# Kernel optimization log

Hardware: AMD Instinct MI355X
Metric: run time of the kernel (lower is better)

Reference implementation:

```python
import jax, jax.numpy as jnp
import numpy as np

NUM_SEM, MAXPP, FS, FG, H, ITERS, ETN, GROUPS = 24, 10, 128, 128, 128, 2, 4, 16
N_NODES, N_EDGES = 20000, 320000


def _leaky(x):
    return jax.nn.leaky_relu(x, 0.01)


def _lin_init(k, din, dout):
    kw, kb = jax.random.split(k)
    lim = 1.0 / np.sqrt(din)
    w = jax.random.uniform(kw, (dout, din), jnp.float32, -lim, lim)
    b = jax.random.uniform(kb, (dout,), jnp.float32, -lim, lim)
    return w, b


def setup_inputs() -> dict:
    key = jax.random.key(0)
    ks = jax.random.split(key, 16)
    inp = {}
    inp["child_feats"] = jax.random.normal(ks[0], (1, N_NODES, NUM_SEM + MAXPP + FS), jnp.float32)
    inp["child_geo_feats"] = jax.random.normal(ks[1], (1, N_NODES, FG), jnp.float32)
    inp["child_exists"] = jnp.ones((1, N_NODES, 1), jnp.float32)
    inp["edge_type_onehot"] = jax.random.uniform(ks[2], (1, N_EDGES, ETN), jnp.float32)
    inp["edge_indices"] = jax.random.randint(ks[3], (1, N_EDGES, 2), 0, N_NODES)
    inp["child_op_w"], inp["child_op_b"] = _lin_init(ks[4], NUM_SEM + MAXPP + FS, H)
    inp["second_w"], inp["second_b"] = _lin_init(ks[5], H * (ITERS + 1), FS)
    ew, eb = zip(*[_lin_init(ks[6 + i], 2 * H + ETN, H) for i in range(ITERS)])
    inp["edge_w"] = jnp.stack(ew)
    inp["edge_b"] = jnp.stack(eb)
    inp["child_geo_w"], inp["child_geo_b"] = _lin_init(ks[10], FG, H)
    inp["second_geo_w"], inp["second_geo_b"] = _lin_init(ks[11], H, FG)
    inp["gn_w"] = jnp.ones((FG,), jnp.float32)
    inp["gn_b"] = jnp.zeros((FG,), jnp.float32)
    inp["skip_w"], inp["skip_b"] = _lin_init(ks[12], FG, FG)
    return inp


def _group_norm(x, w, b, groups=GROUPS, eps=1e-5):
    # x: [B, C]  (torch GroupNorm on 2D input)
    B, C = x.shape
    xg = x.reshape(B, groups, C // groups)
    mu = xg.mean(axis=-1, keepdims=True)
    var = xg.var(axis=-1, keepdims=True)
    xn = ((xg - mu) * jax.lax.rsqrt(var + eps)).reshape(B, C)
    return xn * w + b


def reference(child_feats, child_geo_feats, child_exists, edge_type_onehot, edge_indices,
              child_op_w, child_op_b, second_w, second_b, edge_w, edge_b,
              child_geo_w, child_geo_b, second_geo_w, second_geo_b, gn_w, gn_b, skip_w, skip_b):
    B, N, _ = child_feats.shape
    # struct branch
    cf = (child_feats @ child_op_w.T + child_op_b) * child_exists  # [B,N,H]
    iter_parent_feats = [cf.max(axis=1)]                           # symmetric_type='max'
    idx_from = edge_indices[0, :, 0]
    idx_to = edge_indices[0, :, 1]
    ef = edge_type_onehot[0]                                       # [E,ETN]
    for i in range(ITERS):
        # gather endpoints, concat edge type, edge-MLP + leaky relu
        msg = jnp.concatenate([cf[0, idx_from], cf[0, idx_to], ef], axis=1)  # [E,2H+ETN]
        msg = _leaky(msg @ edge_w[i].T + edge_b[i])                          # [E,H]
        # scatter_max into zero-initialized node slots (matches torch_scatter with out=zeros)
        cf = jnp.zeros((N, H), msg.dtype).at[idx_from].max(msg)[None]        # [1,N,H]
        iter_parent_feats.append(cf.max(axis=1))
    parent_feat = _leaky(jnp.concatenate(iter_parent_feats, axis=1) @ second_w.T + second_b)
    # geo branch
    skip = (child_geo_feats @ skip_w.T + skip_b) * child_exists    # [B,N,FG]
    cg = (child_geo_feats @ child_geo_w.T + child_geo_b) * child_exists  # [B,N,H]
    pg = _leaky(cg.max(axis=1))
    sg = _leaky(skip.max(axis=1))
    parent_geo_feat = _leaky(sg + _group_norm(pg @ second_geo_w.T + second_geo_b, gn_w, gn_b))
    return parent_feat, parent_geo_feat
```

## Files before the change

kernel.cpp:

```cpp
#include <hip/hip_runtime.h>

#define N_NODES 20000
#define N_EDGES 320000
#define HD 128
#define FIN 162
#define KE 260
#define KPAD 288
#define KOP 192
#define WSTR 296
#define OSTR 200
#define GSTR 136
#define TSTR 136
#define XSTR 72

typedef unsigned short u16;
typedef __attribute__((ext_vector_type(8))) short bf16x8;
typedef __attribute__((ext_vector_type(4))) float f32x4;

__device__ __forceinline__ float leaky(float x){ return x > 0.f ? x : 0.01f*x; }
__device__ __forceinline__ unsigned fmap(float f){
    unsigned u = __float_as_uint(f);
    return (u & 0x80000000u) ? ~u : (u | 0x80000000u);
}
__device__ __forceinline__ float funmap(unsigned u){
    return __uint_as_float((u & 0x80000000u) ? (u & 0x7fffffffu) : ~u);
}
__device__ __forceinline__ unsigned umax_(unsigned a, unsigned b){ return a > b ? a : b; }
__device__ __forceinline__ u16 f2bf(float x){
    unsigned b = __float_as_uint(x);
    return (u16)((b + 0x7fffu + ((b >> 16) & 1u)) >> 16);
}
__device__ __forceinline__ float bf2f(u16 u){
    return __uint_as_float(((unsigned)u) << 16);
}

#define PB_W 16
#define PB_F 960
#define PB_G 640
#define PB_H 320
#define PREP_GRID (PB_W + PB_F + PB_G + PB_H)

__global__ __launch_bounds__(256) void prep(
    const float* __restrict__ edge_w, u16* __restrict__ Wb,
    const float* __restrict__ op_w,   u16* __restrict__ Wop,
    const float* __restrict__ geo_w,  u16* __restrict__ Wgeo,
    const float* __restrict__ skip_w, u16* __restrict__ Wskip,
    const float* __restrict__ feats,  u16* __restrict__ featsb,
    const float* __restrict__ geof,   u16* __restrict__ geob,
    const int* __restrict__ eidx, int* __restrict__ count)
{
    const int b = blockIdx.x, t = threadIdx.x;
    if (b < PB_W) {
        for (int idx = b * 256 + t; idx < 16384; idx += PB_W * 256) {
            union { u16 us[8]; uint4 v; } pk;
            if (idx < 9216) {
                int layer = idx / 4608, rem = idx - layer * 4608;
                int h = rem / 36, j = rem - h * 36;
                const float* src = edge_w + (size_t)layer * 128 * KE + h * KE;
                #pragma unroll
                for (int kk = 0; kk < 8; ++kk) {
                    int k = j * 8 + kk;
                    pk.us[kk] = (k < KE) ? f2bf(src[k]) : (u16)0;
                }
                ((uint4*)Wb)[(size_t)layer * 128 * 36 + h * 36 + j] = pk.v;
            } else if (idx < 12288) {
                int rem = idx - 9216;
                int h = rem / 24, j = rem - h * 24;
                const float* src = op_w + h * FIN;
                #pragma unroll
                for (int kk = 0; kk < 8; ++kk) {
                    int k = j * 8 + kk;
                    pk.us[kk] = (k < FIN) ? f2bf(src[k]) : (u16)0;
                }
                ((uint4*)Wop)[h * 24 + j] = pk.v;
            } else {
                int rem = idx - 12288;
                int which = rem >> 11;
                int r2 = rem & 2047;
                const float4* src = (const float4*)((which ? skip_w : geo_w)) + r2 * 2;
                float4 a = src[0], c = src[1];
                pk.us[0]=f2bf(a.x); pk.us[1]=f2bf(a.y); pk.us[2]=f2bf(a.z); pk.us[3]=f2bf(a.w);
                pk.us[4]=f2bf(c.x); pk.us[5]=f2bf(c.y); pk.us[6]=f2bf(c.z); pk.us[7]=f2bf(c.w);
                ((uint4*)(which ? Wskip : Wgeo))[r2] = pk.v;
            }
        }
    } else if (b < PB_W + PB_F) {
        for (int f = (b - PB_W) * 256 + t; f < N_NODES * 24; f += PB_F * 256) {
            int n = f / 24, j = f - n * 24;
            union { u16 us[8]; uint4 v; } pk;
            if (j < 20) {
                const float2* src = (const float2*)(feats + (size_t)n * FIN + j * 8);
                float2 p0 = src[0], p1 = src[1], p2 = src[2], p3 = src[3];
                pk.us[0]=f2bf(p0.x); pk.us[1]=f2bf(p0.y); pk.us[2]=f2bf(p1.x); pk.us[3]=f2bf(p1.y);
                pk.us[4]=f2bf(p2.x); pk.us[5]=f2bf(p2.y); pk.us[6]=f2bf(p3.x); pk.us[7]=f2bf(p3.y);
            } else if (j == 20) {
                float2 p = *(const float2*)(feats + (size_t)n * FIN + 160);
                pk.us[0]=f2bf(p.x); pk.us[1]=f2bf(p.y);
                pk.us[2]=pk.us[3]=pk.us[4]=pk.us[5]=pk.us[6]=pk.us[7]=0;
            } else {
                #pragma unroll
                for (int kk = 0; kk < 8; ++kk) pk.us[kk] = 0;
            }
            ((uint4*)featsb)[(size_t)n * 24 + j] = pk.v;
        }
    } else if (b < PB_W + PB_F + PB_G) {
        for (int g = (b - PB_W - PB_F) * 256 + t; g < N_NODES * 16; g += PB_G * 256) {
            const float4* s = (const float4*)geof + (size_t)g * 2;
            float4 a = s[0], c = s[1];
            union { u16 us[8]; uint4 v; } pk;
            pk.us[0]=f2bf(a.x); pk.us[1]=f2bf(a.y); pk.us[2]=f2bf(a.z); pk.us[3]=f2bf(a.w);
            pk.us[4]=f2bf(c.x); pk.us[5]=f2bf(c.y); pk.us[6]=f2bf(c.z); pk.us[7]=f2bf(c.w);
            ((uint4*)geob)[g] = pk.v;
        }
    } else {
        for (int e = (b - PB_W - PB_F - PB_G) * 256 + t; e < N_EDGES; e += PB_H * 256)
            atomicAdd(&count[eidx[2 * e]], 1);
    }
}

__global__ __launch_bounds__(1024) void scan_offsets(
    const int* __restrict__ count, int* __restrict__ offset)
{
    __shared__ int part[1024];
    const int t = threadIdx.x;
    const int lo = t * 20;
    const int hi = min(lo + 20, N_NODES);
    int s = 0;
    for (int n = lo; n < hi; ++n) s += count[n];
    part[t] = s;
    __syncthreads();
    for (int d = 1; d < 1024; d <<= 1) {
        int v = (t >= d) ? part[t - d] : 0;
        __syncthreads();
        part[t] += v;
        __syncthreads();
    }
    int run = (t > 0) ? part[t - 1] : 0;
    for (int n = lo; n < hi; ++n) { offset[n] = run; run += count[n]; }
}

__global__ __launch_bounds__(256) void mid(
    const int* __restrict__ eidx, const float* __restrict__ ef,
    const int* __restrict__ offset, int* __restrict__ cursor,
    int* __restrict__ from_p, int* __restrict__ to_p, uint2* __restrict__ efb_p,
    const u16* __restrict__ featsb, const u16* __restrict__ geob,
    const float* __restrict__ exists,
    const u16* __restrict__ Wop, const float* __restrict__ op_b,
    const u16* __restrict__ Wgeo, const float* __restrict__ geo_b,
    const u16* __restrict__ Wskip, const float* __restrict__ skip_b,
    u16* __restrict__ cf_a,
    unsigned* __restrict__ ipf0_m, unsigned* __restrict__ pg_m,
    unsigned* __restrict__ sg_m)
{
    __shared__ __align__(16) u16 smem[128 * OSTR];
    __shared__ float ex_s[128];
    __shared__ unsigned colmax_s[128];

    const int blk = blockIdx.x, t = threadIdx.x;
    if (blk < 1250) {
        int e = blk * 256 + t;
        int2 p = ((const int2*)eidx)[e];
        int pos = offset[p.x] + atomicAdd(&cursor[p.x], 1);
        from_p[pos] = p.x; to_p[pos] = p.y;
        float4 e4 = ((const float4*)ef)[e];
        efb_p[pos] = make_uint2(
            (unsigned)f2bf(e4.x) | ((unsigned)f2bf(e4.y) << 16),
            (unsigned)f2bf(e4.z) | ((unsigned)f2bf(e4.w) << 16));
        return;
    }
    const int b = blk - 1250;
    const int mode = (b < 157) ? 0 : (b < 314) ? 1 : 2;
    const int bx = b - (mode == 0 ? 0 : mode == 1 ? 157 : 314);
    const int base = bx * 128;
    const int wave = t >> 6, l = t & 63;
    const int quad = l >> 4, lc = l & 15;
    const int R0 = (wave >> 1) * 64;
    const int C0 = (wave & 1) * 64;

    const u16* W = (mode == 0) ? Wop : (mode == 1) ? Wgeo : Wskip;
    const float* bias = (mode == 0) ? op_b : (mode == 1) ? geo_b : skip_b;
    unsigned* accout = (mode == 0) ? ipf0_m : (mode == 1) ? pg_m : sg_m;
    const int KW = (mode == 0) ? KOP : HD;
    const int SW = (mode == 0) ? OSTR : GSTR;
    const int NCH = (mode == 0) ? 6 : 4;
    const u16* A = (mode == 0) ? featsb : geob;

    {
        const int r = t >> 1, half = t & 1;
        const int nu4 = KW / 16;
        const uint4* src = (const uint4*)(W + (size_t)r * KW) + half * nu4;
        uint4* dst = (uint4*)(smem + r * SW) + half * nu4;
        for (int i = 0; i < nu4; ++i) dst[i] = src[i];
    }
    if (t < 128) {
        int n = base + t; if (n >= N_NODES) n = N_NODES - 1;
        ex_s[t] = exists[n];
        colmax_s[t] = 0u;
    }
    __syncthreads();

    f32x4 acc[4][4];
    #pragma unroll
    for (int i = 0; i < 4; ++i)
        #pragma unroll
        for (int j = 0; j < 4; ++j) acc[i][j] = (f32x4){0.f, 0.f, 0.f, 0.f};

    int nd[4];
    #pragma unroll
    for (int ti = 0; ti < 4; ++ti) {
        int n = base + R0 + ti * 16 + lc;
        nd[ti] = (n < N_NODES) ? n : N_NODES - 1;
    }

    for (int c = 0; c < NCH; ++c) {
        bf16x8 af[4], bfr[4];
        #pragma unroll
        for (int ti = 0; ti < 4; ++ti)
            af[ti] = *(const bf16x8*)(A + (size_t)nd[ti] * KW + c * 32 + quad * 8);
        #pragma unroll
        for (int tj = 0; tj < 4; ++tj)
            bfr[tj] = *(const bf16x8*)(smem + (C0 + tj * 16 + lc) * SW + c * 32 + quad * 8);
        #pragma unroll
        for (int ti = 0; ti < 4; ++ti)
            #pragma unroll
            for (int tj = 0; tj < 4; ++tj)
                acc[ti][tj] = __builtin_amdgcn_mfma_f32_16x16x32_bf16(
                    af[ti], bfr[tj], acc[ti][tj], 0, 0, 0);
    }

    #pragma unroll
    for (int tj = 0; tj < 4; ++tj) {
        const int col = C0 + tj * 16 + lc;
        const float bc = bias[col];
        unsigned mx = 0u;
        #pragma unroll
        for (int ti = 0; ti < 4; ++ti) {
            #pragma unroll
            for (int r = 0; r < 4; ++r) {
                int row = R0 + ti * 16 + quad * 4 + r;
                float x = (acc[ti][tj][r] + bc) * ex_s[row];
                acc[ti][tj][r] = x;
                mx = umax_(mx, fmap(x));
            }
        }
        atomicMax(&colmax_s[col], mx);
    }
    __syncthreads();
    if (t < 128) atomicMax(&accout[t], colmax_s[t]);

    if (mode == 0) {
        #pragma unroll
        for (int ti = 0; ti < 4; ++ti)
            #pragma unroll
            for (int tj = 0; tj < 4; ++tj) {
                const int col = C0 + tj * 16 + lc;
                #pragma unroll
                for (int r = 0; r < 4; ++r)
                    smem[(R0 + ti * 16 + quad * 4 + r) * TSTR + col] = f2bf(acc[ti][tj][r]);
            }
        __syncthreads();
        #pragma unroll
        for (int i = 0; i < 8; ++i) {
            int idx = t + i * 256;
            int row = idx >> 4, c16 = idx & 15;
            int n = base + row;
            if (n < N_NODES) {
                uint4 v = *(const uint4*)(smem + row * TSTR + c16 * 8);
                *(uint4*)(cf_a + (size_t)n * HD + c16 * 8) = v;
            }
        }
    }
}

template<int REDUCE>
__global__ __launch_bounds__(512, 4) void edge_mfma(
    const u16* __restrict__ cfb,
    const int* __restrict__ from_p,
    const int* __restrict__ to_p,
    const uint2* __restrict__ efb_p,
    const u16* __restrict__ Wb,
    const float* __restrict__ bias,
    const int* __restrict__ offs,
    const int* __restrict__ cnt,
    u16* __restrict__ cf_bb,
    float* __restrict__ cf_b32,
    int* __restrict__ ipf_out)
{
    __shared__ __align__(16) u16 smem[64 * WSTR];
    __shared__ int colmax_s[64];

    const int t    = threadIdx.x;
    const int tile = blockIdx.x >> 1;
    const int half = blockIdx.x & 1;
    const int base = tile * 512;
    const int wave = t >> 6, l = t & 63;
    const int quad = l >> 4, lc = l & 15;
    const int R0 = wave * 64;
    const int C0 = half * 64;

    for (int idx = t; idx < 64 * 36; idx += 512) {
        int r = idx / 36, j = idx - r * 36;
        ((uint4*)(smem + r * WSTR))[j] = ((const uint4*)(Wb + (size_t)(C0 + r) * KPAD))[j];
    }
    if (t < 64) colmax_s[t] = 0;

    int nf[4], nt[4]; uint2 efr[4];
    #pragma unroll
    for (int ti = 0; ti < 4; ++ti) {
        int e = base + R0 + ti * 16 + lc;
        nf[ti]  = from_p[e];
        nt[ti]  = to_p[e];
        efr[ti] = efb_p[e];
    }
    __syncthreads();

    f32x4 acc[4][4];
    #pragma unroll
    for (int i = 0; i < 4; ++i)
        #pragma unroll
        for (int j = 0; j < 4; ++j) acc[i][j] = (f32x4){0.f, 0.f, 0.f, 0.f};

    #pragma unroll
    for (int c = 0; c < 8; ++c) {
        bf16x8 af[4], bfr[4];
        #pragma unroll
        for (int ti = 0; ti < 4; ++ti) {
            int node = (c < 4) ? nf[ti] : nt[ti];
            af[ti] = *(const bf16x8*)(cfb + node * HD + (c & 3) * 32 + quad * 8);
        }
        #pragma unroll
        for (int tj = 0; tj < 4; ++tj)
            bfr[tj] = *(const bf16x8*)(smem + (tj * 16 + lc) * WSTR + c * 32 + quad * 8);
        #pragma unroll
        for (int ti = 0; ti < 4; ++ti)
            #pragma unroll
            for (int tj = 0; tj < 4; ++tj)
                acc[ti][tj] = __builtin_amdgcn_mfma_f32_16x16x32_bf16(
                    af[ti], bfr[tj], acc[ti][tj], 0, 0, 0);
    }
    {
        bf16x8 af[4], bfr[4];
        #pragma unroll
        for (int ti = 0; ti < 4; ++ti) {
            union { bf16x8 v; unsigned u[4]; } p;
            p.u[0] = efr[ti].x; p.u[1] = efr[ti].y; p.u[2] = 0u; p.u[3] = 0u;
            union { bf16x8 v; unsigned u[4]; } z;
            z.u[0] = z.u[1] = z.u[2] = z.u[3] = 0u;
            af[ti] = (quad == 0) ? p.v : z.v;
        }
        #pragma unroll
        for (int tj = 0; tj < 4; ++tj)
            bfr[tj] = *(const bf16x8*)(smem + (tj * 16 + lc) * WSTR + 8 * 32 + quad * 8);
        #pragma unroll
        for (int ti = 0; ti < 4; ++ti)
            #pragma unroll
            for (int tj = 0; tj < 4; ++tj)
                acc[ti][tj] = __builtin_amdgcn_mfma_f32_16x16x32_bf16(
                    af[ti], bfr[tj], acc[ti][tj], 0, 0, 0);
    }

    #pragma unroll
    for (int tj = 0; tj < 4; ++tj) {
        const int cl = tj * 16 + lc;
        const float bc = bias[C0 + cl];
        float mx = 0.f;
        #pragma unroll
        for (int ti = 0; ti < 4; ++ti) {
            #pragma unroll
            for (int r = 0; r < 4; ++r) {
                float x = leaky(acc[ti][tj][r] + bc);
                acc[ti][tj][r] = x;
                mx = fmaxf(mx, x);
            }
        }
        atomicMax(&colmax_s[cl], __float_as_int(mx));
    }
    __syncthreads();
    if (t < 64) atomicMax(&ipf_out[C0 + t], colmax_s[t]);

    if (REDUCE) {
        const int ch = t & 63;
        #pragma unroll
        for (int ph = 0; ph < 2; ++ph) {
            if ((R0 >> 8) == ph) {
                const int rb = R0 & 255;
                #pragma unroll
                for (int ti = 0; ti < 4; ++ti)
                    #pragma unroll
                    for (int tj = 0; tj < 4; ++tj) {
                        const int cl = tj * 16 + lc;
                        #pragma unroll
                        for (int r = 0; r < 4; ++r)
                            smem[(rb + ti * 16 + quad * 4 + r) * XSTR + cl]
                                = f2bf(acc[ti][tj][r]);
                    }
            }
            __syncthreads();
            const int wb = base + ph * 256;
            const int nfirst = from_p[wb];
            const int nlast  = from_p[wb + 255];
            for (int n = nfirst + (t >> 6); n <= nlast; n += 8) {
                int o = offs[n], c = cnt[n];
                int lo = o - wb, hi = o + c - wb;
                int lo2 = lo > 0 ? lo : 0;
                int hi2 = hi < 256 ? hi : 256;
                if (lo2 >= hi2) continue;
                float m = 0.f;
                for (int r = lo2; r < hi2; ++r)
                    m = fmaxf(m, bf2f(smem[r * XSTR + ch]));
                if (lo >= 0 && hi <= 256)
                    cf_bb[(size_t)n * HD + C0 + ch] = f2bf(m);
                else
                    atomicMax((int*)&cf_b32[(size_t)n * HD + C0 + ch], __float_as_int(m));
            }
            __syncthreads();
        }
    }
}

__global__ __launch_bounds__(256) void fixup(
    const int* __restrict__ offs, const int* __restrict__ cnt,
    const float* __restrict__ cf_b32, u16* __restrict__ cf_bb)
{
    const int n = blockIdx.x * 2 + (threadIdx.x >> 7);
    const int ch = threadIdx.x & 127;
    int o = offs[n], c = cnt[n];
    if (c > 0 && (o >> 8) != ((o + c - 1) >> 8))
        cf_bb[(size_t)n * HD + ch] = f2bf(cf_b32[(size_t)n * HD + ch]);
}

__global__ __launch_bounds__(128) void heads(
    const unsigned* __restrict__ ipf0_m,
    const float* __restrict__ ipf1, const float* __restrict__ ipf2,
    const float* __restrict__ secW, const float* __restrict__ secB,
    const unsigned* __restrict__ pg_m, const unsigned* __restrict__ sg_m,
    const float* __restrict__ geoW, const float* __restrict__ geoB,
    const float* __restrict__ gnw, const float* __restrict__ gnb,
    float* __restrict__ out)
{
    const int t = threadIdx.x;
    if (blockIdx.x == 0) {
        __shared__ float s[384];
        s[t]       = funmap(ipf0_m[t]);
        s[128 + t] = ipf1[t];
        s[256 + t] = ipf2[t];
        __syncthreads();
        float acc = secB[t];
        #pragma unroll 4
        for (int k = 0; k < 384; ++k) acc = fmaf(s[k], secW[t*384 + k], acc);
        out[t] = leaky(acc);
    } else {
        __shared__ float pg[128];
        __shared__ float tt[128];
        pg[t] = leaky(funmap(pg_m[t]));
        float sg = leaky(funmap(sg_m[t]));
        __syncthreads();
        float acc = geoB[t];
        #pragma unroll 4
        for (int k = 0; k < 128; ++k) acc = fmaf(pg[k], geoW[t*128 + k], acc);
        tt[t] = acc;
        __syncthreads();
        const int g = (t >> 3) << 3;
        float mu = 0.f, m2 = 0.f;
        #pragma unroll
        for (int q = 0; q < 8; ++q) { float x = tt[g + q]; mu += x; m2 += x*x; }
        mu *= 0.125f;
        m2 = m2 * 0.125f - mu * mu;
        float xn = (acc - mu) * rsqrtf(m2 + 1e-5f);
        out[128 + t] = leaky(sg + xn * gnw[t] + gnb[t]);
    }
}

extern "C" void kernel_launch(void* const* d_in, const int* in_sizes, int n_in,
                              void* d_out, int out_size, void* d_ws, size_t ws_size,
                              hipStream_t stream)
{
    const float* child_feats  = (const float*)d_in[0];
    const float* child_geo    = (const float*)d_in[1];
    const float* child_exists = (const float*)d_in[2];
    const float* etoh         = (const float*)d_in[3];
    const int*   eidx         = (const int*)  d_in[4];
    const float* op_w   = (const float*)d_in[5];
    const float* op_b   = (const float*)d_in[6];
    const float* sec_w  = (const float*)d_in[7];
    const float* sec_b  = (const float*)d_in[8];
    const float* edge_w = (const float*)d_in[9];
    const float* edge_b = (const float*)d_in[10];
    const float* geo_w  = (const float*)d_in[11];
    const float* geo_b  = (const float*)d_in[12];
    const float* sgeo_w = (const float*)d_in[13];
    const float* sgeo_b = (const float*)d_in[14];
    const float* gn_w   = (const float*)d_in[15];
    const float* gn_b   = (const float*)d_in[16];
    const float* skip_w = (const float*)d_in[17];
    const float* skip_b = (const float*)d_in[18];
    float* out = (float*)d_out;

    char* ws = (char*)d_ws;
    size_t off = 0;
    u16*   cf_a   = (u16*)(ws + off);   off += (size_t)N_NODES*HD*2;
    u16*   featsb = (u16*)(ws + off);   off += (size_t)N_NODES*KOP*2;
    u16*   geob   = (u16*)(ws + off);   off += (size_t)N_NODES*HD*2;
    u16*   Wb     = (u16*)(ws + off);   off += (size_t)2*128*KPAD*2;
    u16*   Wop    = (u16*)(ws + off);   off += (size_t)128*KOP*2;
    u16*   Wgeo   = (u16*)(ws + off);   off += (size_t)128*128*2;
    u16*   Wskip  = (u16*)(ws + off);   off += (size_t)128*128*2;
    int*   from_p = (int*)(ws + off);   off += (size_t)N_EDGES*4;
    int*   to_p   = (int*)(ws + off);   off += (size_t)N_EDGES*4;
    uint2* efb_p  = (uint2*)(ws + off); off += (size_t)N_EDGES*8;
    int*   offs   = (int*)(ws + off);   off += (size_t)N_NODES*4;
    char*  zero0  = ws + off;
    u16*   cf_bb  = (u16*)(ws + off);         off += (size_t)N_NODES*HD*2;
    float* cf_b32 = (float*)(ws + off);       off += (size_t)N_NODES*HD*4;
    unsigned* ipf0_m = (unsigned*)(ws + off); off += 128*4;
    float*    ipf1   = (float*)(ws + off);    off += 128*4;
    float*    ipf2   = (float*)(ws + off);    off += 128*4;
    unsigned* pg_m   = (unsigned*)(ws + off); off += 128*4;
    unsigned* sg_m   = (unsigned*)(ws + off); off += 128*4;
    int*      count  = (int*)(ws + off);      off += (size_t)N_NODES*4;
    int*      cursor = (int*)(ws + off);      off += (size_t)N_NODES*4;
    size_t zero_bytes = (size_t)(ws + off - zero0);

    hipMemsetAsync(zero0, 0, zero_bytes, stream);

    prep<<<PREP_GRID, 256, 0, stream>>>(
        edge_w, Wb, op_w, Wop, geo_w, Wgeo, skip_w, Wskip,
        child_feats, featsb, child_geo, geob, eidx, count);

    scan_offsets<<<1, 1024, 0, stream>>>(count, offs);

    mid<<<1721, 256, 0, stream>>>(
        eidx, etoh, offs, cursor, from_p, to_p, efb_p,
        featsb, geob, child_exists, Wop, op_b, Wgeo, geo_b, Wskip, skip_b,
        cf_a, ipf0_m, pg_m, sg_m);

    edge_mfma<1><<<2 * (N_EDGES/512), 512, 0, stream>>>(
        cf_a, from_p, to_p, efb_p, Wb, edge_b,
        offs, count, cf_bb, cf_b32, (int*)ipf1);

    fixup<<<N_NODES/2, 256, 0, stream>>>(offs, count, cf_b32, cf_bb);

    edge_mfma<0><<<2 * (N_EDGES/512), 512, 0, stream>>>(
        cf_bb, from_p, to_p, efb_p, Wb + 128*KPAD, edge_b + 128,
        offs, count, nullptr, nullptr, (int*)ipf2);

    heads<<<2, 128, 0, stream>>>(ipf0_m, ipf1, ipf2, sec_w, sec_b,
                                 pg_m, sg_m, sgeo_w, sgeo_b, gn_w, gn_b, out);
}
```

Baseline: 294.8 us.

## Compute all 128 output columns per edge block and fold bias into GEMM

Each edge block now computes the full 128 output channels instead of splitting them across two half-blocks, so gathered node rows are loaded and used for MFMA once instead of twice. The bias is folded into the weight matrix as an extra K column, matched by a constant 1.0 in the edge-type fragment, which removes the per-column bias load and add. The scatter-max staging buffer is transposed to channel-major with packed bf16 conversion stores. The trade-off is twice the accumulator registers and shared memory per block, with the occupancy hint lowered from 4 to 2 blocks.

```diff
diff --git a/kernel.cpp b/kernel.cpp
--- a/kernel.cpp
+++ b/kernel.cpp
@@ -11,13 +11,13 @@
 #define OSTR 200
 #define GSTR 136
 #define TSTR 136
-#define XSTR 72
+#define RSTR 260
 
 typedef unsigned short u16;
 typedef __attribute__((ext_vector_type(8))) short bf16x8;
 typedef __attribute__((ext_vector_type(4))) float f32x4;
 
-__device__ __forceinline__ float leaky(float x){ return x > 0.f ? x : 0.01f*x; }
+__device__ __forceinline__ float leaky(float x){ return fmaxf(x, 0.01f*x); }
 __device__ __forceinline__ unsigned fmap(float f){
     unsigned u = __float_as_uint(f);
     return (u & 0x80000000u) ? ~u : (u | 0x80000000u);
@@ -32,6 +32,11 @@
 }
 __device__ __forceinline__ float bf2f(u16 u){
     return __uint_as_float(((unsigned)u) << 16);
+}
+__device__ __forceinline__ unsigned cvt_pk_bf16(float lo, float hi){
+    unsigned r;
+    asm("v_cvt_pk_bf16_f32 %0, %1, %2" : "=v"(r) : "v"(lo), "v"(hi));
+    return r;
 }
 
 #define PB_W 16
@@ -41,7 +46,8 @@
 #define PREP_GRID (PB_W + PB_F + PB_G + PB_H)
 
 __global__ __launch_bounds__(256) void prep(
-    const float* __restrict__ edge_w, u16* __restrict__ Wb,
+    const float* __restrict__ edge_w, const float* __restrict__ edge_bias,
+    u16* __restrict__ Wb,
     const float* __restrict__ op_w,   u16* __restrict__ Wop,
     const float* __restrict__ geo_w,  u16* __restrict__ Wgeo,
     const float* __restrict__ skip_w, u16* __restrict__ Wskip,
@@ -60,7 +66,9 @@
                 #pragma unroll
                 for (int kk = 0; kk < 8; ++kk) {
                     int k = j * 8 + kk;
-                    pk.us[kk] = (k < KE) ? f2bf(src[k]) : (u16)0;
+                    pk.us[kk] = (k < KE) ? f2bf(src[k])
+                              : (k == 260) ? f2bf(edge_bias[layer * 128 + h])
+                              : (u16)0;
                 }
                 ((uint4*)Wb)[(size_t)layer * 128 * 36 + h * 36 + j] = pk.v;
             } else if (idx < 12288) {
@@ -273,36 +281,32 @@
 }
 
 template<int REDUCE>
-__global__ __launch_bounds__(512, 4) void edge_mfma(
+__global__ __launch_bounds__(512, 2) void edge_mfma(
     const u16* __restrict__ cfb,
     const int* __restrict__ from_p,
     const int* __restrict__ to_p,
     const uint2* __restrict__ efb_p,
     const u16* __restrict__ Wb,
-    const float* __restrict__ bias,
     const int* __restrict__ offs,
     const int* __restrict__ cnt,
     u16* __restrict__ cf_bb,
     float* __restrict__ cf_b32,
     int* __restrict__ ipf_out)
 {
-    __shared__ __align__(16) u16 smem[64 * WSTR];
-    __shared__ int colmax_s[64];
+    __shared__ __align__(16) u16 smem[128 * WSTR];
+    __shared__ int colmax_s[128];
 
     const int t    = threadIdx.x;
-    const int tile = blockIdx.x >> 1;
-    const int half = blockIdx.x & 1;
-    const int base = tile * 512;
+    const int base = blockIdx.x * 512;
     const int wave = t >> 6, l = t & 63;
     const int quad = l >> 4, lc = l & 15;
     const int R0 = wave * 64;
-    const int C0 = half * 64;
-
-    for (int idx = t; idx < 64 * 36; idx += 512) {
+
+    for (int idx = t; idx < 128 * 36; idx += 512) {
         int r = idx / 36, j = idx - r * 36;
-        ((uint4*)(smem + r * WSTR))[j] = ((const uint4*)(Wb + (size_t)(C0 + r) * KPAD))[j];
-    }
-    if (t < 64) colmax_s[t] = 0;
+        ((uint4*)(smem + r * WSTR))[j] = ((const uint4*)(Wb + (size_t)r * KPAD))[j];
+    }
+    if (t < 128) colmax_s[t] = 0;
 
     int nf[4], nt[4]; uint2 efr[4];
     #pragma unroll
@@ -314,61 +318,62 @@
     }
     __syncthreads();
 
-    f32x4 acc[4][4];
+    f32x4 acc[4][8];
     #pragma unroll
     for (int i = 0; i < 4; ++i)
         #pragma unroll
-        for (int j = 0; j < 4; ++j) acc[i][j] = (f32x4){0.f, 0.f, 0.f, 0.f};
+        for (int j = 0; j < 8; ++j) acc[i][j] = (f32x4){0.f, 0.f, 0.f, 0.f};
 
     #pragma unroll
     for (int c = 0; c < 8; ++c) {
-        bf16x8 af[4], bfr[4];
+        bf16x8 af[4], bfr[8];
         #pragma unroll
         for (int ti = 0; ti < 4; ++ti) {
             int node = (c < 4) ? nf[ti] : nt[ti];
             af[ti] = *(const bf16x8*)(cfb + node * HD + (c & 3) * 32 + quad * 8);
         }
         #pragma unroll
-        for (int tj = 0; tj < 4; ++tj)
+        for (int tj = 0; tj < 8; ++tj)
             bfr[tj] = *(const bf16x8*)(smem + (tj * 16 + lc) * WSTR + c * 32 + quad * 8);
         #pragma unroll
         for (int ti = 0; ti < 4; ++ti)
             #pragma unroll
-            for (int tj = 0; tj < 4; ++tj)
+            for (int tj = 0; tj < 8; ++tj)
                 acc[ti][tj] = __builtin_amdgcn_mfma_f32_16x16x32_bf16(
                     af[ti], bfr[tj], acc[ti][tj], 0, 0, 0);
     }
     {
-        bf16x8 af[4], bfr[4];
+        bf16x8 af[4], bfr[8];
         #pragma unroll
         for (int ti = 0; ti < 4; ++ti) {
             union { bf16x8 v; unsigned u[4]; } p;
-            p.u[0] = efr[ti].x; p.u[1] = efr[ti].y; p.u[2] = 0u; p.u[3] = 0u;
+            p.u[0] = efr[ti].x; p.u[1] = efr[ti].y;
+            p.u[2] = 0x00003f80u;
+            p.u[3] = 0u;
             union { bf16x8 v; unsigned u[4]; } z;
             z.u[0] = z.u[1] = z.u[2] = z.u[3] = 0u;
             af[ti] = (quad == 0) ? p.v : z.v;
         }
         #pragma unroll
-        for (int tj = 0; tj < 4; ++tj)
+        for (int tj = 0; tj < 8; ++tj)
             bfr[tj] = *(const bf16x8*)(smem + (tj * 16 + lc) * WSTR + 8 * 32 + quad * 8);
         #pragma unroll
         for (int ti = 0; ti < 4; ++ti)
             #pragma unroll
-            for (int tj = 0; tj < 4; ++tj)
+            for (int tj = 0; tj < 8; ++tj)
                 acc[ti][tj] = __builtin_amdgcn_mfma_f32_16x16x32_bf16(
                     af[ti], bfr[tj], acc[ti][tj], 0, 0, 0);
     }
 
     #pragma unroll
-    for (int tj = 0; tj < 4; ++tj) {
+    for (int tj = 0; tj < 8; ++tj) {
         const int cl = tj * 16 + lc;
-        const float bc = bias[C0 + cl];
         float mx = 0.f;
         #pragma unroll
         for (int ti = 0; ti < 4; ++ti) {
             #pragma unroll
             for (int r = 0; r < 4; ++r) {
-                float x = leaky(acc[ti][tj][r] + bc);
+                float x = leaky(acc[ti][tj][r]);
                 acc[ti][tj][r] = x;
                 mx = fmaxf(mx, x);
             }
@@ -376,10 +381,11 @@
         atomicMax(&colmax_s[cl], __float_as_int(mx));
     }
     __syncthreads();
-    if (t < 64) atomicMax(&ipf_out[C0 + t], colmax_s[t]);
+    if (t < 128) atomicMax(&ipf_out[t], colmax_s[t]);
 
     if (REDUCE) {
-        const int ch = t & 63;
+        const int ch  = t & 127;
+        const int grp = t >> 7;
         #pragma unroll
         for (int ph = 0; ph < 2; ++ph) {
             if ((R0 >> 8) == ph) {
@@ -387,19 +393,20 @@
                 #pragma unroll
                 for (int ti = 0; ti < 4; ++ti)
                     #pragma unroll
-                    for (int tj = 0; tj < 4; ++tj) {
+                    for (int tj = 0; tj < 8; ++tj) {
                         const int cl = tj * 16 + lc;
-                        #pragma unroll
-                        for (int r = 0; r < 4; ++r)
-                            smem[(rb + ti * 16 + quad * 4 + r) * XSTR + cl]
-                                = f2bf(acc[ti][tj][r]);
+                        const int rowb = rb + ti * 16 + quad * 4;
+                        uint2 pk;
+                        pk.x = cvt_pk_bf16(acc[ti][tj][0], acc[ti][tj][1]);
+                        pk.y = cvt_pk_bf16(acc[ti][tj][2], acc[ti][tj][3]);
+                        *(uint2*)(smem + cl * RSTR + rowb) = pk;
                     }
             }
             __syncthreads();
             const int wb = base + ph * 256;
             const int nfirst = from_p[wb];
             const int nlast  = from_p[wb + 255];
-            for (int n = nfirst + (t >> 6); n <= nlast; n += 8) {
+            for (int n = nfirst + grp; n <= nlast; n += 4) {
                 int o = offs[n], c = cnt[n];
                 int lo = o - wb, hi = o + c - wb;
                 int lo2 = lo > 0 ? lo : 0;
@@ -407,11 +414,11 @@
                 if (lo2 >= hi2) continue;
                 float m = 0.f;
                 for (int r = lo2; r < hi2; ++r)
-                    m = fmaxf(m, bf2f(smem[r * XSTR + ch]));
+                    m = fmaxf(m, bf2f(smem[ch * RSTR + r]));
                 if (lo >= 0 && hi <= 256)
-                    cf_bb[(size_t)n * HD + C0 + ch] = f2bf(m);
+                    cf_bb[(size_t)n * HD + ch] = f2bf(m);
                 else
-                    atomicMax((int*)&cf_b32[(size_t)n * HD + C0 + ch], __float_as_int(m));
+                    atomicMax((int*)&cf_b32[(size_t)n * HD + ch], __float_as_int(m));
             }
             __syncthreads();
         }
@@ -524,7 +531,7 @@
     hipMemsetAsync(zero0, 0, zero_bytes, stream);
 
     prep<<<PREP_GRID, 256, 0, stream>>>(
-        edge_w, Wb, op_w, Wop, geo_w, Wgeo, skip_w, Wskip,
+        edge_w, edge_b, Wb, op_w, Wop, geo_w, Wgeo, skip_w, Wskip,
         child_feats, featsb, child_geo, geob, eidx, count);
 
     scan_offsets<<<1, 1024, 0, stream>>>(count, offs);
@@ -534,14 +541,14 @@
         featsb, geob, child_exists, Wop, op_b, Wgeo, geo_b, Wskip, skip_b,
         cf_a, ipf0_m, pg_m, sg_m);
 
-    edge_mfma<1><<<2 * (N_EDGES/512), 512, 0, stream>>>(
-        cf_a, from_p, to_p, efb_p, Wb, edge_b,
+    edge_mfma<1><<<N_EDGES/512, 512, 0, stream>>>(
+        cf_a, from_p, to_p, efb_p, Wb,
         offs, count, cf_bb, cf_b32, (int*)ipf1);
 
     fixup<<<N_NODES/2, 256, 0, stream>>>(offs, count, cf_b32, cf_bb);
 
-    edge_mfma<0><<<2 * (N_EDGES/512), 512, 0, stream>>>(
-        cf_bb, from_p, to_p, efb_p, Wb + 128*KPAD, edge_b + 128,
+    edge_mfma<0><<<N_EDGES/512, 512, 0, stream>>>(
+        cf_bb, from_p, to_p, efb_p, Wb + 128*KPAD,
         offs, count, nullptr, nullptr, (int*)ipf2);
 
     heads<<<2, 128, 0, stream>>>(ipf0_m, ipf1, ipf2, sec_w, sec_b,
```

Result: slower. 307.5 us (+4.3%).
